# Optimization experiments

Hardware: AMD Instinct MI355X
Metric: run time of the kernel (lower is better)

## Reference

```python
import jax, jax.numpy as jnp
import numpy as np

THRESHOLD = 0.299
WS = 16  # window_size


def setup_inputs() -> dict:
    key = jax.random.key(0)
    k1, k2, k3 = jax.random.split(key, 3)
    B, D, H = 64, 1536, 384
    N = WS * WS  # 256 windows -> h_inputs second dim
    return {
        "input_features": jax.random.normal(k1, (B, D), dtype=jnp.float32),
        "h_inputs": jax.random.normal(k2, (B, N, D), dtype=jnp.float32),
        "preds": jax.random.normal(k3, (B, 1, H, H), dtype=jnp.float32),
    }


def reference(input_features, h_inputs, preds):
    # --- entropy of predicted probabilities ---
    if bool(jnp.all((preds >= 0) & (preds <= 1))):
        probs = preds
    else:
        probs = jax.nn.sigmoid(preds)
    entropy = -probs * jnp.log(jnp.clip(probs, 1e-5))  # [B,1,H,W]

    # --- adaptive_avg_pool2d to (WS, WS); H,W divisible by WS so it's mean pooling ---
    B, C, H, W = entropy.shape
    scores = entropy.astype(jnp.float32).reshape(
        B, C, WS, H // WS, WS, W // WS).mean(axis=(3, 5))  # [B,1,WS,WS]
    mask = scores > THRESHOLD  # [B,1,WS,WS]

    # --- window_sets: gather high-entropy window features, repeat image features ---
    flat_mask = mask.reshape(-1)                 # [B*WS*WS]
    num = mask.reshape(B, -1).sum(axis=1)        # windows selected per image
    h_input_features = h_inputs.reshape(B * WS * WS, -1)[flat_mask]   # [K, D]
    l_input_features = jnp.repeat(input_features, num, axis=0,
                                  total_repeat_length=int(num.sum()))  # [K, D]

    # --- get_position: (y,x) coords of selected windows, concatenated over batch ---
    gy, gx = jnp.meshgrid(jnp.arange(WS), jnp.arange(WS), indexing='ij')
    coords = jnp.stack([gy, gx], axis=-1).reshape(-1, 2)   # [WS*WS, 2]
    coords_list = jnp.tile(coords, (B, 1))[flat_mask]      # [K, 2]

    return (l_input_features, h_input_features, mask, coords_list, entropy)
```

## Files before the change

### kernel.cpp

```cpp
#include <hip/hip_runtime.h>
#include <math.h>

constexpr int B     = 64;
constexpr int D     = 1536;
constexpr int H     = 384;
constexpr int WS    = 16;
constexpr int NW    = WS * WS;
constexpr int SUB   = H / WS;
constexpr int IMG   = H * H;
constexpr int TOT   = B * IMG;
constexpr int TOTW  = B * NW;
constexpr int NBAND = B * WS;

__device__ __forceinline__ float sig_entropy_f(float x) {
    float p  = 1.0f / (1.0f + __expf(-x));
    float pc = p < 1e-5f ? 1e-5f : p;
    return -p * __logf(pc);
}

__device__ __forceinline__ double sig_entropy_d(double x) {
    double p  = 1.0 / (1.0 + exp(-x));
    double pc = p < 1e-5 ? 1e-5 : p;
    return (double)(float)(-p * log(pc));
}

__global__ __launch_bounds__(384, 3) void fused_kernel(
        const float* __restrict__ preds,
        float* __restrict__ ent,
        float* __restrict__ maskOut,
        unsigned char* __restrict__ flags) {
    __shared__ double part[384];
    __shared__ double warr[6];
    __shared__ int    bflag[16];

    const int band = blockIdx.x;
    const int b    = band >> 4;
    const int wy   = band & 15;
    const int t    = threadIdx.x;
    const int lane = t & 63;
    const int wv   = t >> 6;
    const int g    = t % 96;
    const int rr   = t / 96;

    const float4* p4 = (const float4*)preds;
    float4*       e4 = (float4*)ent;
    size_t base4 = ((size_t)b * IMG + (size_t)(wy * SUB) * H) / 4 + g;

    double s = 0.0;
#pragma unroll
    for (int k = 0; k < 6; ++k) {
        size_t idx = base4 + (size_t)(rr + 4 * k) * (H / 4);
        float4 v = p4[idx];
        float e0 = sig_entropy_f(v.x);
        float e1 = sig_entropy_f(v.y);
        float e2 = sig_entropy_f(v.z);
        float e3 = sig_entropy_f(v.w);
        e4[idx] = make_float4(e0, e1, e2, e3);
        s += (double)e0 + (double)e1 + (double)e2 + (double)e3;
    }
    part[t] = s;
    __syncthreads();

    if (t < WS) {
        double tot = 0.0;
        for (int rr2 = 0; rr2 < 4; ++rr2)
            for (int g2 = 0; g2 < 6; ++g2)
                tot += part[rr2 * 96 + t * 6 + g2];
        float score = (float)(tot / 576.0);
        float d = score - 0.299f;
        int sel = d > 0.0f ? 1 : 0;
        int w = b * NW + wy * WS + t;
        flags[w]   = (unsigned char)sel;
        maskOut[w] = sel ? 1.0f : 0.0f;
        bflag[t]   = (fabsf(d) < 1e-4f) ? 1 : 0;
    }
    __syncthreads();

    for (int wx = 0; wx < WS; ++wx) {
        if (!bflag[wx]) continue;
        const float* basep = preds + (size_t)b * IMG
                           + (size_t)(wy * SUB) * H + wx * SUB;
        int r0 = t / SUB, c0 = t % SUB;
        double sd = sig_entropy_d((double)basep[r0 * H + c0]);
        if (t < 192) {
            int e2i = t + 384;
            int r1 = e2i / SUB, c1 = e2i % SUB;
            sd += sig_entropy_d((double)basep[r1 * H + c1]);
        }
        for (int off = 32; off > 0; off >>= 1)
            sd += __shfl_down(sd, off, 64);
        if (lane == 0) warr[wv] = sd;
        __syncthreads();
        if (t == 0) {
            double tot = 0.0;
            for (int i = 0; i < 6; ++i) tot += warr[i];
            float score = (float)(tot / 576.0);
            int sel = (score > 0.299f) ? 1 : 0;
            int w = b * NW + wy * WS + wx;
            flags[w]   = (unsigned char)sel;
            maskOut[w] = sel ? 1.0f : 0.0f;
        }
        __syncthreads();
    }
}

__global__ __launch_bounds__(384) void scan_gather_kernel(
        const float* __restrict__ inF,
        const float* __restrict__ hIn,
        const unsigned char* __restrict__ flags,
        float* __restrict__ outL,
        float* __restrict__ outH,
        float* __restrict__ coords) {
    __shared__ uint4 flv[TOTW / 16];
    __shared__ int   cpref[257];
    __shared__ int   wsum4[4];
    __shared__ int   woff4[4];
    __shared__ int   sw;

    unsigned char* fl = (unsigned char*)flv;
    const int t    = threadIdx.x;
    const int lane = t & 63;
    const int wv   = t >> 6;

    for (int j = t; j < TOTW / 16; j += 384)
        flv[j] = ((const uint4*)flags)[j];
    __syncthreads();

    int partial = 0;
    if (t < 256) {
        const unsigned int* p = (const unsigned int*)(fl + t * 64);
#pragma unroll
        for (int j = 0; j < 16; ++j) {
            unsigned int wd = p[j];
            partial += (int)(((wd & 0x01010101u) * 0x01010101u) >> 24);
        }
    }
    int x = partial;
#pragma unroll
    for (int off = 1; off < 64; off <<= 1) {
        int y = __shfl_up(x, off, 64);
        if (lane >= off) x += y;
    }
    if (t < 256 && lane == 63) wsum4[wv] = x;
    __syncthreads();
    if (t == 0) {
        int a = 0;
        for (int i = 0; i < 4; ++i) { woff4[i] = a; a += wsum4[i]; }
        cpref[256] = a;
    }
    __syncthreads();
    if (t < 256) cpref[t] = woff4[wv] + x - partial;
    __syncthreads();

    const int Kv = cpref[256];
    for (int k = blockIdx.x; k < Kv; k += gridDim.x) {
        if (t == 0) {
            int lo = 0, hi = 255;
            while (lo < hi) {
                int mid = (lo + hi + 1) >> 1;
                if (cpref[mid] <= k) lo = mid; else hi = mid - 1;
            }
            int r = k - cpref[lo];
            int basei = lo * 64;
            int w = basei;
            for (int j = 0; j < 64; ++j) {
                if (fl[basei + j]) {
                    if (r == 0) { w = basei + j; break; }
                    --r;
                }
            }
            sw = w;
        }
        __syncthreads();
        const int w  = sw;
        const int b  = w >> 8;
        const int wi = w & 255;
        const float4* src_h = (const float4*)(hIn + (size_t)w * D);
        const float4* src_l = (const float4*)(inF + (size_t)b * D);
        float4* dst_h = (float4*)(outH + (size_t)k * D);
        float4* dst_l = (float4*)(outL + (size_t)k * D);
        dst_h[t] = src_h[t];
        dst_l[t] = src_l[t];
        if (t == 0) {
            coords[2 * (size_t)k]     = (float)(wi >> 4);
            coords[2 * (size_t)k + 1] = (float)(wi & 15);
        }
        __syncthreads();
    }
}

extern "C" void kernel_launch(void* const* d_in, const int* in_sizes, int n_in,
                              void* d_out, int out_size, void* d_ws, size_t ws_size,
                              hipStream_t stream) {
    const float* input_features = (const float*)d_in[0];
    const float* h_inputs       = (const float*)d_in[1];
    const float* preds          = (const float*)d_in[2];
    float* out = (float*)d_out;

    int K = (out_size - TOT - TOTW) / (2 * D + 2);
    float* outL      = out;
    float* outH      = out + (size_t)K * D;
    float* outMask   = out + (size_t)2 * K * D;
    float* outCoords = outMask + TOTW;
    float* outEnt    = outCoords + (size_t)2 * K;

    unsigned char* flags = (unsigned char*)d_ws;

    fused_kernel<<<NBAND, 384, 0, stream>>>(preds, outEnt, outMask, flags);
    scan_gather_kernel<<<1024, 384, 0, stream>>>(input_features, h_inputs, flags,
                                                 outL, outH, outCoords);
}
```

Before: 73.87 us.

## Use nontemporal loads/stores and precompute selected-window list in shared memory

After: 81.35 us. +10.1%, slower.

```diff
diff --git a/kernel.cpp b/kernel.cpp
--- a/kernel.cpp
+++ b/kernel.cpp
@@ -12,6 +12,8 @@
 constexpr int TOTW  = B * NW;
 constexpr int NBAND = B * WS;
 
+typedef float v4f __attribute__((ext_vector_type(4)));
+
 __device__ __forceinline__ float sig_entropy_f(float x) {
     float p  = 1.0f / (1.0f + __expf(-x));
     float pc = p < 1e-5f ? 1e-5f : p;
@@ -42,21 +44,22 @@
     const int g    = t % 96;
     const int rr   = t / 96;
 
-    const float4* p4 = (const float4*)preds;
-    float4*       e4 = (float4*)ent;
+    const v4f* p4 = (const v4f*)preds;
+    v4f*       e4 = (v4f*)ent;
     size_t base4 = ((size_t)b * IMG + (size_t)(wy * SUB) * H) / 4 + g;
 
     double s = 0.0;
 #pragma unroll
     for (int k = 0; k < 6; ++k) {
         size_t idx = base4 + (size_t)(rr + 4 * k) * (H / 4);
-        float4 v = p4[idx];
-        float e0 = sig_entropy_f(v.x);
-        float e1 = sig_entropy_f(v.y);
-        float e2 = sig_entropy_f(v.z);
-        float e3 = sig_entropy_f(v.w);
-        e4[idx] = make_float4(e0, e1, e2, e3);
-        s += (double)e0 + (double)e1 + (double)e2 + (double)e3;
+        v4f v = __builtin_nontemporal_load(&p4[idx]);
+        v4f e;
+        e.x = sig_entropy_f(v.x);
+        e.y = sig_entropy_f(v.y);
+        e.z = sig_entropy_f(v.z);
+        e.w = sig_entropy_f(v.w);
+        __builtin_nontemporal_store(e, &e4[idx]);
+        s += (double)e.x + (double)e.y + (double)e.z + (double)e.w;
     }
     part[t] = s;
     __syncthreads();
@@ -111,28 +114,28 @@
         float* __restrict__ outL,
         float* __restrict__ outH,
         float* __restrict__ coords) {
-    __shared__ uint4 flv[TOTW / 16];
-    __shared__ int   cpref[257];
-    __shared__ int   wsum4[4];
-    __shared__ int   woff4[4];
-    __shared__ int   sw;
+    __shared__ uint4          flv[TOTW / 16];
+    __shared__ unsigned short lst[TOTW];
+    __shared__ int            wsum4[4];
+    __shared__ int            woff4[4];
+    __shared__ int            Ktot;
 
     unsigned char* fl = (unsigned char*)flv;
     const int t    = threadIdx.x;
     const int lane = t & 63;
     const int wv   = t >> 6;
 
-    for (int j = t; j < TOTW / 16; j += 384)
-        flv[j] = ((const uint4*)flags)[j];
-    __syncthreads();
-
     int partial = 0;
     if (t < 256) {
-        const unsigned int* p = (const unsigned int*)(fl + t * 64);
+        const uint4* f4 = (const uint4*)flags;
 #pragma unroll
-        for (int j = 0; j < 16; ++j) {
-            unsigned int wd = p[j];
-            partial += (int)(((wd & 0x01010101u) * 0x01010101u) >> 24);
+        for (int j = 0; j < 4; ++j) {
+            uint4 r = f4[t * 4 + j];
+            flv[t * 4 + j] = r;
+            partial += (int)(((r.x & 0x01010101u) * 0x01010101u) >> 24);
+            partial += (int)(((r.y & 0x01010101u) * 0x01010101u) >> 24);
+            partial += (int)(((r.z & 0x01010101u) * 0x01010101u) >> 24);
+            partial += (int)(((r.w & 0x01010101u) * 0x01010101u) >> 24);
         }
     }
     int x = partial;
@@ -146,46 +149,35 @@
     if (t == 0) {
         int a = 0;
         for (int i = 0; i < 4; ++i) { woff4[i] = a; a += wsum4[i]; }
-        cpref[256] = a;
-    }
-    __syncthreads();
-    if (t < 256) cpref[t] = woff4[wv] + x - partial;
-    __syncthreads();
-
-    const int Kv = cpref[256];
+        Ktot = a;
+    }
+    __syncthreads();
+    if (t < 256) {
+        int o    = woff4[wv] + x - partial;
+        int base = t * 64;
+        for (int j = 0; j < 64; ++j) {
+            if (fl[base + j]) lst[o++] = (unsigned short)(base + j);
+        }
+    }
+    __syncthreads();
+
+    const int Kv = Ktot;
+    const v4f* inF4 = (const v4f*)inF;
     for (int k = blockIdx.x; k < Kv; k += gridDim.x) {
-        if (t == 0) {
-            int lo = 0, hi = 255;
-            while (lo < hi) {
-                int mid = (lo + hi + 1) >> 1;
-                if (cpref[mid] <= k) lo = mid; else hi = mid - 1;
-            }
-            int r = k - cpref[lo];
-            int basei = lo * 64;
-            int w = basei;
-            for (int j = 0; j < 64; ++j) {
-                if (fl[basei + j]) {
-                    if (r == 0) { w = basei + j; break; }
-                    --r;
-                }
-            }
-            sw = w;
-        }
-        __syncthreads();
-        const int w  = sw;
+        const int w  = lst[k];
         const int b  = w >> 8;
         const int wi = w & 255;
-        const float4* src_h = (const float4*)(hIn + (size_t)w * D);
-        const float4* src_l = (const float4*)(inF + (size_t)b * D);
-        float4* dst_h = (float4*)(outH + (size_t)k * D);
-        float4* dst_l = (float4*)(outL + (size_t)k * D);
-        dst_h[t] = src_h[t];
-        dst_l[t] = src_l[t];
+        const v4f* src_h = (const v4f*)(hIn + (size_t)w * D);
+        v4f* dst_h = (v4f*)(outH + (size_t)k * D);
+        v4f* dst_l = (v4f*)(outL + (size_t)k * D);
+        v4f hv = __builtin_nontemporal_load(&src_h[t]);
+        v4f lv = inF4[(size_t)b * (D / 4) + t];
+        __builtin_nontemporal_store(hv, &dst_h[t]);
+        __builtin_nontemporal_store(lv, &dst_l[t]);
         if (t == 0) {
             coords[2 * (size_t)k]     = (float)(wi >> 4);
             coords[2 * (size_t)k + 1] = (float)(wi & 15);
         }
-        __syncthreads();
     }
 }
 
```
